# Optimization experiments

Hardware: AMD Instinct MI355X
Metric: run time of the kernel (lower is better)

The kernel has to match this reference:

```python
import jax, jax.numpy as jnp
import numpy as np

B, S, D = 4, 1024, 768
H = 12
DK = D // H            # 64
NUM_EMB = 10
MAX_DIST = 100000.0 * 2 ** 0.5
POS_SCALE = 100000.0   # tile positions live in [0, 100000]


def setup_inputs() -> dict:
    key = jax.random.key(0)
    ks = jax.random.split(key, 12)
    query = jax.random.normal(ks[0], (B, S, D), dtype=jnp.float32)
    key_t = jax.random.normal(ks[1], (B, S, D), dtype=jnp.float32)
    value = jax.random.normal(ks[2], (B, S, D), dtype=jnp.float32)
    tile_positions = jax.random.uniform(ks[3], (B, S, 2), dtype=jnp.float32) * POS_SCALE
    # Linear weights, torch layout [out, in]; xavier_uniform init, zero bias
    lim = float(np.sqrt(6.0 / (D + D)))
    Wq = jax.random.uniform(ks[4], (D, D), minval=-lim, maxval=lim, dtype=jnp.float32)
    Wk = jax.random.uniform(ks[5], (D, D), minval=-lim, maxval=lim, dtype=jnp.float32)
    Wv = jax.random.uniform(ks[6], (D, D), minval=-lim, maxval=lim, dtype=jnp.float32)
    bq = jnp.zeros((D,), jnp.float32)
    bk = jnp.zeros((D,), jnp.float32)
    bv = jnp.zeros((D,), jnp.float32)
    emb_k = jax.random.normal(ks[7], (NUM_EMB, DK), dtype=jnp.float32)  # nn.Embedding default N(0,1)
    return {"query": query, "key": key_t, "value": value,
            "tile_positions": tile_positions,
            "Wq": Wq, "bq": bq, "Wk": Wk, "bk": bk, "Wv": Wv, "bv": bv,
            "emb_k": emb_k}


def reference(query, key, value, tile_positions, Wq, bq, Wk, bk, Wv, bv, emb_k):
    b, s, _ = query.shape
    # projections -> [B, H, S, DK]
    q = (query @ Wq.T + bq).reshape(b, s, H, DK).transpose(0, 2, 1, 3)
    k = (key   @ Wk.T + bk).reshape(b, s, H, DK).transpose(0, 2, 1, 3)
    v = (value @ Wv.T + bv).reshape(b, s, H, DK).transpose(0, 2, 1, 3)
    # pairwise distances, normalized, discretized to embedding indices
    pos = jax.lax.stop_gradient(tile_positions)
    diff = pos[:, :, None, :] - pos[:, None, :, :]          # [B,S,S,2]
    dist = jnp.sqrt(jnp.sum(diff * diff, axis=-1)) / MAX_DIST  # [B,S,S]
    idx = jnp.clip(jnp.round(dist * (NUM_EMB - 1)), 0, NUM_EMB - 1).astype(jnp.int32)
    rk = emb_k[idx]                                          # [B,S,S,DK]
    # logits: QK^T plus distance-aware key bias
    attn_logits = jnp.einsum('bhqd,bhkd->bhqk', q, k)
    attn_logits = attn_logits + jnp.einsum('bhqd,bqkd->bhqk', q, rk)
    attn_logits = attn_logits / (DK ** 0.5)
    attention = jax.nn.softmax(attn_logits, axis=-1)
    out = jnp.einsum('bhqk,bhkd->bhqd', attention, v)       # [B,H,S,DK]
    out = out.transpose(0, 2, 1, 3).reshape(b, s, -1)       # [B,S,D]
    return out
```

## Files before the change

kernel.cpp:

```cpp
#include <hip/hip_runtime.h>
#include <hip/hip_bf16.h>

#define Bsz 4
#define Ssz 1024
#define Dsz 768
#define Hn 12
#define DKsz 64
#define NUMEMB 10

#define IDX_OFF 64
#define K_OFF   4194368
#define V_OFF   10485824
#define WBF_OFF 16777280
#define XBF_OFF 20316224
#define WS_TIER_B 20316224ULL
#define WS_TIER_A 39190592ULL

#define NXz 3145728
#define NWz 589824

#define KVBUF 4096

typedef __attribute__((ext_vector_type(8))) short short8;
typedef __attribute__((ext_vector_type(8))) float float8;
typedef __attribute__((ext_vector_type(4))) float f32x4;
typedef __attribute__((ext_vector_type(4))) unsigned int u32x4;
typedef __attribute__((ext_vector_type(2))) unsigned int u32x2;
typedef __attribute__((ext_vector_type(4))) short s16x4;

__device__ __forceinline__ float bfbits2f(short u) {
    union { unsigned int i; float f; } v;
    v.i = ((unsigned int)(unsigned short)u) << 16;
    return v.f;
}
__device__ __forceinline__ unsigned short f2bf_bits(float f) {
    __hip_bfloat16 h = __float2bfloat16(f);
    return *reinterpret_cast<unsigned short*>(&h);
}

__device__ __forceinline__ int dtvote(const unsigned int* p, int n) {
    int cnt = 0;
    for (int i = (threadIdx.x & 63); i < n; i += 64) {
        const unsigned int ex = (p[i] >> 7) & 0xFF;
        cnt += (ex >= 110 && ex <= 145) ? 1 : 0;
    }
#pragma unroll
    for (int off = 1; off < 64; off <<= 1) cnt += __shfl_xor(cnt, off, 64);
    return (2 * cnt > n) ? 1 : 0;
}

template<bool BF16>
__device__ __forceinline__ float loadf(const void* base, size_t idx) {
    if constexpr (BF16) return __bfloat162float(((const __hip_bfloat16*)base)[idx]);
    else return ((const float*)base)[idx];
}
template<bool BF16>
__device__ __forceinline__ short8 load8bf(const void* base, size_t idx) {
    if constexpr (BF16) {
        return *(const short8*)((const short*)base + idx);
    } else {
        float8 f = *(const float8*)((const float*)base + idx);
        short8 r;
#pragma unroll
        for (int i = 0; i < 8; i++) r[i] = (short)f2bf_bits(f[i]);
        return r;
    }
}
template<bool BF16>
__device__ __forceinline__ float8 load8f(const void* base, size_t idx) {
    if constexpr (BF16) {
        short8 s = *(const short8*)((const short*)base + idx);
        float8 f;
#pragma unroll
        for (int i = 0; i < 8; i++) f[i] = bfbits2f(s[i]);
        return f;
    } else {
        return *(const float8*)((const float*)base + idx);
    }
}

template<bool PB>
__device__ __forceinline__ void idx_body(
    const void* pos, unsigned char* __restrict__ idxb, int kt, int qt, int b)
{
    const int t = threadIdx.x;
    const int r = t >> 2, cc = t & 3;
    const int q = qt * 64 + r;
    const float qx = loadf<PB>(pos, ((size_t)b * Ssz + q) * 2);
    const float qy = loadf<PB>(pos, ((size_t)b * Ssz + q) * 2 + 1);
    const float MAXD = 141421.35623730951f;
    const int k0 = kt * 64 + cc * 16;
    unsigned int w[4];
#pragma unroll
    for (int g = 0; g < 4; g++) {
        unsigned int acc = 0;
#pragma unroll
        for (int u = 0; u < 4; u++) {
            const int k = k0 + g * 4 + u;
            const float kx = loadf<PB>(pos, ((size_t)b * Ssz + k) * 2);
            const float ky = loadf<PB>(pos, ((size_t)b * Ssz + k) * 2 + 1);
            const float dx = __fsub_rn(qx, kx);
            const float dy = __fsub_rn(qy, ky);
            const float ss = __fadd_rn(__fmul_rn(dx, dx), __fmul_rn(dy, dy));
            const float dist = __fdiv_rn(sqrtf(ss), MAXD);
            const float d9 = __fmul_rn(dist, 9.0f);
            int idx = (int)rintf(d9);
            idx = idx < 0 ? 0 : (idx > NUMEMB - 1 ? NUMEMB - 1 : idx);
            acc |= ((unsigned int)idx) << (8 * u);
        }
        w[g] = acc;
    }
    u32x4 v; v[0] = w[0]; v[1] = w[1]; v[2] = w[2]; v[3] = w[3];
    *(u32x4*)(idxb + ((size_t)(b * Ssz + q)) * Ssz + k0) = v;
}

__global__ __launch_bounds__(64) void detect_kernel(
    const unsigned int* __restrict__ q, const unsigned int* __restrict__ p,
    const unsigned int* __restrict__ w, const unsigned int* __restrict__ e,
    int* __restrict__ flags)
{
    const int which = blockIdx.x;
    const unsigned int* ptr = (which == 0) ? q : ((which == 1) ? p : ((which == 2) ? w : e));
    const int n = (which == 3) ? 320 : ((which == 1) ? 4096 : 1024);
    const int f = dtvote(ptr, n);
    if (threadIdx.x == 0) flags[which] = f;
}

__global__ __launch_bounds__(256) void idx_kernel(
    const void* pos, const int* __restrict__ flags, unsigned char* __restrict__ idxb)
{
    if (flags[1] != 0) idx_body<true >(pos, idxb, blockIdx.x, blockIdx.y, blockIdx.z);
    else               idx_body<false>(pos, idxb, blockIdx.x, blockIdx.y, blockIdx.z);
}

__global__ __launch_bounds__(256) void prep_kernel(
    const void* __restrict__ X0, const void* __restrict__ X1, const void* __restrict__ X2,
    const void* __restrict__ W0, const void* __restrict__ W1, const void* __restrict__ W2,
    const void* __restrict__ tpos, const void* __restrict__ emb,
    int* __restrict__ flags, short* __restrict__ Xbf, short* __restrict__ Wbf,
    unsigned char* __restrict__ idxb, int nconv, int doX)
{
    if ((int)blockIdx.x >= nconv) {
        const int i = blockIdx.x - nconv;
        const int kt = i & 15, qt = (i >> 4) & 15, b = i >> 8;
        const int pb = dtvote((const unsigned int*)tpos, 1024);
        if (pb) idx_body<true >(tpos, idxb, kt, qt, b);
        else    idx_body<false>(tpos, idxb, kt, qt, b);
        return;
    }

    if (blockIdx.x == 1) {
        const int f = dtvote((const unsigned int*)tpos, 1024);
        if (threadIdx.x == 0) flags[1] = f;
    } else if (blockIdx.x == 3) {
        const int f = dtvote((const unsigned int*)emb, 320);
        if (threadIdx.x == 0) flags[3] = f;
    }
    const bool xb = dtvote((const unsigned int*)X0, 256) != 0;
    const bool wb = dtvote((const unsigned int*)W0, 256) != 0;
    if (blockIdx.x == 0 && threadIdx.x == 0) { flags[0] = xb ? 1 : 0; flags[2] = wb ? 1 : 0; }

    const long t = (long)blockIdx.x * 256 + threadIdx.x;
    if (doX) {
        const long i8 = t * 8;
        if (i8 < (long)3 * NXz) {
            const int z = (int)(i8 / NXz);
            const long off = i8 - (long)z * NXz;
            const void* X = (z == 0) ? X0 : ((z == 1) ? X1 : X2);
            short8 v = xb ? load8bf<true>(X, off) : load8bf<false>(X, off);
            *(short8*)(Xbf + i8) = v;
        } else {
            const long j = i8 - (long)3 * NXz;
            const int z = (int)(j / NWz);
            const long off = j - (long)z * NWz;
            const void* W = (z == 0) ? W0 : ((z == 1) ? W1 : W2);
            short8 v = wb ? load8bf<true>(W, off) : load8bf<false>(W, off);
            *(short8*)(Wbf + j) = v;
        }
    } else {
        const long j = t * 8;
        const int z = (int)(j / NWz);
        const long off = j - (long)z * NWz;
        const void* W = (z == 0) ? W0 : ((z == 1) ? W1 : W2);
        short8 v = wb ? load8bf<true>(W, off) : load8bf<false>(W, off);
        *(short8*)(Wbf + j) = v;
    }
}

template<bool XB, bool WB>
__device__ __forceinline__ void proj_body(
    const void* X, const void* W, const void* bias, bool biasbf, void* Y, bool ybf,
    int zmode, int bx, int by, short* As, short* Bs)
{
    const int tid  = threadIdx.x;
    const int wave = tid >> 6;
    const int lane = tid & 63;
    const int l15  = lane & 15;
    const int quad = lane >> 4;
    const int wm = wave & 1;
    const int wn = wave >> 1;
    const int m0 = bx * 64;
    const int n0 = by * 128;

    f32x4 acc[2][4];
#pragma unroll
    for (int i = 0; i < 2; i++)
#pragma unroll
        for (int j = 0; j < 4; j++) acc[i][j] = (f32x4)0.0f;

    const int r0 = tid >> 3;
    const int cc = tid & 7;

    short8 pa0 = load8bf<XB>(X, (size_t)(m0 + r0)      * Dsz + cc * 8);
    short8 pa1 = load8bf<XB>(X, (size_t)(m0 + 32 + r0) * Dsz + cc * 8);
    short8 pb0 = load8bf<WB>(W, (size_t)(n0 + r0)      * Dsz + cc * 8);
    short8 pb1 = load8bf<WB>(W, (size_t)(n0 + 32 + r0) * Dsz + cc * 8);
    short8 pb2 = load8bf<WB>(W, (size_t)(n0 + 64 + r0) * Dsz + cc * 8);
    short8 pb3 = load8bf<WB>(W, (size_t)(n0 + 96 + r0) * Dsz + cc * 8);

    for (int kk = 0; kk < Dsz; kk += 64) {
        __syncthreads();
        *(short8*)&As[(r0)      * 72 + cc * 8] = pa0;
        *(short8*)&As[(32 + r0) * 72 + cc * 8] = pa1;
        *(short8*)&Bs[(r0)      * 72 + cc * 8] = pb0;
        *(short8*)&Bs[(32 + r0) * 72 + cc * 8] = pb1;
        *(short8*)&Bs[(64 + r0) * 72 + cc * 8] = pb2;
        *(short8*)&Bs[(96 + r0) * 72 + cc * 8] = pb3;
        __syncthreads();

        if (kk + 64 < Dsz) {
            const int k2 = kk + 64 + cc * 8;
            pa0 = load8bf<XB>(X, (size_t)(m0 + r0)      * Dsz + k2);
            pa1 = load8bf<XB>(X, (size_t)(m0 + 32 + r0) * Dsz + k2);
            pb0 = load8bf<WB>(W, (size_t)(n0 + r0)      * Dsz + k2);
            pb1 = load8bf<WB>(W, (size_t)(n0 + 32 + r0) * Dsz + k2);
            pb2 = load8bf<WB>(W, (size_t)(n0 + 64 + r0) * Dsz + k2);
            pb3 = load8bf<WB>(W, (size_t)(n0 + 96 + r0) * Dsz + k2);
        }

#pragma unroll
        for (int st = 0; st < 2; st++) {
            short8 af[2], bf[4];
#pragma unroll
            for (int i = 0; i < 2; i++)
                af[i] = *(const short8*)&As[(wm * 32 + i * 16 + l15) * 72 + st * 32 + quad * 8];
#pragma unroll
            for (int j = 0; j < 4; j++)
                bf[j] = *(const short8*)&Bs[(wn * 64 + j * 16 + l15) * 72 + st * 32 + quad * 8];
#pragma unroll
            for (int i = 0; i < 2; i++)
#pragma unroll
                for (int j = 0; j < 4; j++)
                    acc[i][j] = __builtin_amdgcn_mfma_f32_16x16x32_bf16(af[i], bf[j], acc[i][j], 0, 0, 0);
        }
    }

#pragma unroll
    for (int j = 0; j < 4; j++) {
        const int n = n0 + wn * 64 + j * 16 + l15;
        const float bv_ = biasbf ? loadf<true>(bias, n) : loadf<false>(bias, n);
        const int hh = n >> 6, dk = n & 63;
#pragma unroll
        for (int i = 0; i < 2; i++) {
            const int ms = m0 + wm * 32 + i * 16 + quad * 4;
            const int bb = ms >> 10;
            const int s0 = ms & 1023;
            if (zmode == 2) {
                s16x4 pkv;
#pragma unroll
                for (int r = 0; r < 4; r++) pkv[r] = (short)f2bf_bits(acc[i][j][r] + bv_);
                *(s16x4*)((short*)Y + (((size_t)bb * Hn + hh) * DKsz + dk) * Ssz + s0) = pkv;
            } else if (zmode == 1) {
#pragma unroll
                for (int r = 0; r < 4; r++)
                    ((__hip_bfloat16*)Y)[(((size_t)bb * Hn + hh) * Ssz + (s0 + r)) * DKsz + dk] =
                        __float2bfloat16(acc[i][j][r] + bv_);
            } else {
#pragma unroll
                for (int r = 0; r < 4; r++) {
                    const float val = acc[i][j][r] + bv_;
                    const size_t oi = (size_t)(ms + r) * Dsz + n;
                    if (ybf) ((__hip_bfloat16*)Y)[oi] = __float2bfloat16(val);
                    else     ((float*)Y)[oi] = val;
                }
            }
        }
    }
}

__global__ __launch_bounds__(256) void proj_kernel(
    const void* X0, const void* X1, const void* X2,
    const void* Wq, const void* bq, const void* Wk, const void* bk,
    const void* Wv, const void* bv,
    void* Qw, void* Kw, void* Vw, const int* __restrict__ flags,
    int fx, int fw)
{
    __shared__ __align__(16) short As[64 * 72];
    __shared__ __align__(16) short Bs[128 * 72];
    const int z = blockIdx.z;
    const void* X = (z == 0) ? X0 : ((z == 1) ? X1 : X2);
    const void* W = (z == 0) ? Wq : ((z == 1) ? Wk : Wv);
    const void* B = (z == 0) ? bq : ((z == 1) ? bk : bv);
    void* Y = (z == 0) ? Qw : ((z == 1) ? Kw : Vw);
    const bool xb = fx || flags[0] != 0;
    const bool wb = fw || flags[2] != 0;
    const bool biasbf = flags[2] != 0;
    const bool ybf = (flags[0] != 0) || (z != 0);
    if (xb) { if (wb) proj_body<true , true >(X, W, B, biasbf, Y, ybf, z, blockIdx.x, blockIdx.y, As, Bs);
              else    proj_body<true , false>(X, W, B, biasbf, Y, ybf, z, blockIdx.x, blockIdx.y, As, Bs); }
    else    { if (wb) proj_body<false, true >(X, W, B, biasbf, Y, ybf, z, blockIdx.x, blockIdx.y, As, Bs);
              else    proj_body<false, false>(X, W, B, biasbf, Y, ybf, z, blockIdx.x, blockIdx.y, As, Bs); }
}

template<bool QB, bool EB>
__device__ __forceinline__ void attn_body(
    const void* Qw, const short* __restrict__ Ks, const short* __restrict__ Vs,
    const unsigned char* __restrict__ idxb, const void* __restrict__ emb, void* out,
    unsigned short* Klds, unsigned short* Vtlds, float* qe)
{
    const int qt = blockIdx.x, h = blockIdx.y, b = blockIdx.z;
    const int tid  = threadIdx.x;
    const int wave = tid >> 6;
    const int lane = tid & 63;
    const int l15  = lane & 15;
    const int quad = lane >> 4;

    const float CSC = 0.18033688011112042f;

    for (int p = tid; p < 64 * NUMEMB; p += 256) {
        const int row = p / NUMEMB, e = p - row * NUMEMB;
        const size_t qoff = ((size_t)b * Ssz + qt * 64 + row) * Dsz + h * DKsz;
        float s = 0.f;
#pragma unroll
        for (int c = 0; c < 8; c++) {
            short8 qv = load8bf<QB>(Qw, qoff + c * 8);
            float8 ef = load8f<EB>(emb, (size_t)e * DKsz + c * 8);
#pragma unroll
            for (int i = 0; i < 8; i++) s += bfbits2f(qv[i]) * ef[i];
        }
        qe[p] = s * CSC;
    }

    short8 qfrag[2];
    {
        const size_t qbase = ((size_t)b * Ssz + qt * 64 + wave * 16 + l15) * Dsz + h * DKsz;
        qfrag[0] = load8bf<QB>(Qw, qbase + quad * 8);
        qfrag[1] = load8bf<QB>(Qw, qbase + 32 + quad * 8);
    }

    float m_run = -1e30f, l_run = 0.f;
    f32x4 oacc[4];
#pragma unroll
    for (int j = 0; j < 4; j++) oacc[j] = (f32x4)0.0f;

    const int r0 = tid >> 3, cc = tid & 7;
    const int swr   = (r0 & 3) | (((r0 >> 3) & 1) << 2);
    const int wroff = r0 * 64 + (cc ^ swr) * 8;

    const int swk = (l15 & 3) | (((l15 >> 2) & 1) << 2);
    const int vsw = (l15 & 3) | (((l15 >> 3) & 1) << 2);
    int koff[4][2];
#pragma unroll
    for (int jb = 0; jb < 4; jb++) {
        const int krow = (jb & 2) * 16 + (l15 >> 2) * 8 + (jb & 1) * 4 + (l15 & 3);
#pragma unroll
        for (int st = 0; st < 2; st++)
            koff[jb][st] = krow * 64 + ((st * 4 + quad) ^ swk) * 8;
    }
    int voff[2];
#pragma unroll
    for (int st = 0; st < 2; st++) voff[st] = ((st * 4 + quad) ^ vsw) * 8;

    const short* kp = Ks + ((size_t)(b * Hn + h) * Ssz) * DKsz + tid * 8;
    const short* vp = Vs + ((size_t)(b * Hn + h) * DKsz + r0) * Ssz + cc * 8;
    const unsigned char* ip = idxb + ((size_t)b * Ssz + qt * 64 + wave * 16 + l15) * Ssz + quad * 8;
    const int qrow10 = (wave * 16 + l15) * NUMEMB;

    short8 pk0 = *(const short8*)(kp);
    short8 pk1 = *(const short8*)(kp + 2048);
    short8 pv0 = *(const short8*)(vp);
    short8 pv1 = *(const short8*)(vp + 32 * Ssz);
    u32x2 idA = *(const u32x2*)(ip);
    u32x2 idB = *(const u32x2*)(ip + 32);

    *(short8*)&Klds[wroff]            = pk0;
    *(short8*)&Klds[32 * 64 + wroff]  = pk1;
    *(short8*)&Vtlds[wroff]           = pv0;
    *(short8*)&Vtlds[32 * 64 + wroff] = pv1;
    __syncthreads();

    for (int it = 0; it < 16; ++it) {
        const int cur = (it & 1) * KVBUF;
        const int nxt = cur ^ KVBUF;
        const unsigned int jd[4] = { idA[0], idA[1], idB[0], idB[1] };

        if (it + 1 < 16) {
            kp += 4096;
            vp += 64;
            ip += 64;
            pk0 = *(const short8*)(kp);
            pk1 = *(const short8*)(kp + 2048);
            pv0 = *(const short8*)(vp);
            pv1 = *(const short8*)(vp + 32 * Ssz);
            idA = *(const u32x2*)(ip);
            idB = *(const u32x2*)(ip + 32);
        }

        f32x4 sf[4];
#pragma unroll
        for (int jb = 0; jb < 4; jb++) sf[jb] = (f32x4)0.0f;
        __builtin_amdgcn_s_setprio(1);
#pragma unroll
        for (int st = 0; st < 2; st++) {
#pragma unroll
            for (int jb = 0; jb < 4; jb++) {
                short8 kf = *(const short8*)&Klds[cur + koff[jb][st]];
                sf[jb] = __builtin_amdgcn_mfma_f32_16x16x32_bf16(kf, qfrag[st], sf[jb], 0, 0, 0);
            }
        }
        __builtin_amdgcn_s_setprio(0);

        float sv[4][4];
#pragma unroll
        for (int jb = 0; jb < 4; jb++) {
            const unsigned int iw = jd[jb];
#pragma unroll
            for (int r = 0; r < 4; r++)
                sv[jb][r] = fmaf(sf[jb][r], CSC, qe[qrow10 + ((iw >> (8 * r)) & 0xFF)]);
        }

        float t0 = fmaxf(fmaxf(sv[0][0], sv[0][1]), fmaxf(sv[0][2], sv[0][3]));
        float t1 = fmaxf(fmaxf(sv[1][0], sv[1][1]), fmaxf(sv[1][2], sv[1][3]));
        float t2 = fmaxf(fmaxf(sv[2][0], sv[2][1]), fmaxf(sv[2][2], sv[2][3]));
        float t3 = fmaxf(fmaxf(sv[3][0], sv[3][1]), fmaxf(sv[3][2], sv[3][3]));
        float vmax = fmaxf(fmaxf(t0, t1), fmaxf(t2, t3));
        vmax = fmaxf(vmax, __shfl_xor(vmax, 16, 64));
        vmax = fmaxf(vmax, __shfl_xor(vmax, 32, 64));

        if (!__all(vmax - m_run <= 8.0f)) {
            const float mnew = fmaxf(m_run, vmax);
            const float alpha = exp2f(m_run - mnew);
            m_run = mnew;
            l_run *= alpha;
            float aO[4];
#pragma unroll
            for (int r = 0; r < 4; r++)
                aO[r] = __shfl(alpha, (lane & 48) | (quad * 4 + r), 64);
#pragma unroll
            for (int j = 0; j < 4; j++) {
                f32x4 o = oacc[j];
#pragma unroll
                for (int r = 0; r < 4; r++) o[r] *= aO[r];
                oacc[j] = o;
            }
        }

#pragma unroll
        for (int jb = 0; jb < 4; jb++)
#pragma unroll
            for (int r = 0; r < 4; r++)
                sv[jb][r] = exp2f(sv[jb][r] - m_run);

        float s0 = (sv[0][0] + sv[0][1]) + (sv[0][2] + sv[0][3]);
        float s1 = (sv[1][0] + sv[1][1]) + (sv[1][2] + sv[1][3]);
        float s2 = (sv[2][0] + sv[2][1]) + (sv[2][2] + sv[2][3]);
        float s3 = (sv[3][0] + sv[3][1]) + (sv[3][2] + sv[3][3]);
        float psum = (s0 + s1) + (s2 + s3);
        psum += __shfl_xor(psum, 16, 64);
        psum += __shfl_xor(psum, 32, 64);
        l_run += psum;

        short8 pa[2];
#pragma unroll
        for (int st = 0; st < 2; st++)
#pragma unroll
            for (int j = 0; j < 8; j++)
                pa[st][j] = (short)f2bf_bits(sv[2 * st + (j >> 2)][j & 3]);

        __builtin_amdgcn_s_setprio(1);
#pragma unroll
        for (int st = 0; st < 2; st++) {
#pragma unroll
            for (int j = 0; j < 4; j++) {
                short8 vb = *(const short8*)&Vtlds[cur + (j * 16 + l15) * 64 + voff[st]];
                oacc[j] = __builtin_amdgcn_mfma_f32_16x16x32_bf16(pa[st], vb, oacc[j], 0, 0, 0);
            }
        }
        __builtin_amdgcn_s_setprio(0);

        if (it + 1 < 16) {
            *(short8*)&Klds[nxt + wroff]            = pk0;
            *(short8*)&Klds[nxt + 32 * 64 + wroff]  = pk1;
            *(short8*)&Vtlds[nxt + wroff]           = pv0;
            *(short8*)&Vtlds[nxt + 32 * 64 + wroff] = pv1;
        }
        __syncthreads();
    }

    const float inv = 1.0f / l_run;
    float invO[4];
#pragma unroll
    for (int r = 0; r < 4; r++)
        invO[r] = __shfl(inv, (lane & 48) | (quad * 4 + r), 64);

#pragma unroll
    for (int r = 0; r < 4; r++) {
        const int m = qt * 64 + wave * 16 + quad * 4 + r;
#pragma unroll
        for (int j = 0; j < 4; j++) {
            const int n = h * DKsz + j * 16 + l15;
            const float val = oacc[j][r] * invO[r];
            const size_t oidx = ((size_t)b * Ssz + m) * Dsz + n;
            if constexpr (QB) ((__hip_bfloat16*)out)[oidx] = __float2bfloat16(val);
            else              ((float*)out)[oidx] = val;
        }
    }
}

__global__ __launch_bounds__(256) void attn_kernel(
    const void* Qw, const short* __restrict__ Ks, const short* __restrict__ Vs,
    const unsigned char* __restrict__ idxb, const void* __restrict__ emb, void* out,
    const int* __restrict__ flags)
{
    __shared__ __align__(16) unsigned short Klds[2 * KVBUF];
    __shared__ __align__(16) unsigned short Vtlds[2 * KVBUF];
    __shared__ __align__(16) float qe[64 * NUMEMB];

    const bool qb = flags[0] != 0, eb = flags[3] != 0;
    if (qb) { if (eb) attn_body<true , true >(Qw, Ks, Vs, idxb, emb, out, Klds, Vtlds, qe);
              else    attn_body<true , false>(Qw, Ks, Vs, idxb, emb, out, Klds, Vtlds, qe); }
    else    { if (eb) attn_body<false, true >(Qw, Ks, Vs, idxb, emb, out, Klds, Vtlds, qe);
              else    attn_body<false, false>(Qw, Ks, Vs, idxb, emb, out, Klds, Vtlds, qe); }
}

extern "C" void kernel_launch(void* const* d_in, const int* in_sizes, int n_in,
                              void* d_out, int out_size, void* d_ws, size_t ws_size,
                              hipStream_t stream) {
    const void* query = d_in[0];
    const void* key   = d_in[1];
    const void* value = d_in[2];
    const void* tpos  = d_in[3];
    const void* Wq    = d_in[4];
    const void* bq    = d_in[5];
    const void* Wk    = d_in[6];
    const void* bk    = d_in[7];
    const void* Wv    = d_in[8];
    const void* bv    = d_in[9];
    const void* emb   = d_in[10];

    int*           flags = (int*)d_ws;
    unsigned char* idxb  = (unsigned char*)d_ws + IDX_OFF;
    void*          Kw    = (char*)d_ws + K_OFF;
    void*          Vw    = (char*)d_ws + V_OFF;
    short*         Wbf   = (short*)((char*)d_ws + WBF_OFF);
    short*         Xbf   = (short*)((char*)d_ws + XBF_OFF);
    void*          Qw    = d_out;

    const bool tierA = ws_size >= WS_TIER_A;
    const bool tierB = !tierA && ws_size >= WS_TIER_B;

    if (tierA) {
        prep_kernel<<<5472 + 1024, 256, 0, stream>>>(
            query, key, value, Wq, Wk, Wv, tpos, emb,
            flags, Xbf, Wbf, idxb, 5472, 1);
        proj_kernel<<<dim3(64, 6, 3), 256, 0, stream>>>(
            Xbf, Xbf + NXz, Xbf + 2 * NXz,
            Wbf, bq, Wbf + NWz, bk, Wbf + 2 * NWz, bv,
            Qw, Kw, Vw, flags, 1, 1);
    } else if (tierB) {
        prep_kernel<<<864 + 1024, 256, 0, stream>>>(
            query, key, value, Wq, Wk, Wv, tpos, emb,
            flags, Xbf, Wbf, idxb, 864, 0);
        proj_kernel<<<dim3(64, 6, 3), 256, 0, stream>>>(
            query, key, value,
            Wbf, bq, Wbf + NWz, bk, Wbf + 2 * NWz, bv,
            Qw, Kw, Vw, flags, 0, 1);
    } else {
        detect_kernel<<<4, 64, 0, stream>>>(
            (const unsigned int*)query, (const unsigned int*)tpos,
            (const unsigned int*)Wq, (const unsigned int*)emb, flags);
        idx_kernel<<<dim3(16, 16, Bsz), 256, 0, stream>>>(tpos, flags, idxb);
        proj_kernel<<<dim3(64, 6, 3), 256, 0, stream>>>(
            query, key, value, Wq, bq, Wk, bk, Wv, bv,
            Qw, Kw, Vw, flags, 0, 0);
    }

    attn_kernel<<<dim3(16, Hn, Bsz), 256, 0, stream>>>(
        Qw, (const short*)Kw, (const short*)Vw, idxb, emb, d_out, flags);
}
```

Measured before the change: 201.4 us.

## Enlarge attention query tile to 128 rows with 512-thread blocks

Each attention block now covers 128 query rows using 8 waves and 512 threads, which halves the grid. Every K/V tile staged in shared memory is therefore reused by twice as many query rows, and each thread issues one K and one V load per iteration instead of two. The cost is fewer blocks for the GPU, less parallelism, and heavier register pressure under the 512-thread launch bound. The code still uses `tid>>3` row mapping with 512 threads, so r0 now spans 0..63, and the K/V tile layout must remain consistent with that mapping.

```diff
diff --git a/kernel.cpp b/kernel.cpp
--- a/kernel.cpp
+++ b/kernel.cpp
@@ -20,6 +20,7 @@
 #define NWz 589824
 
 #define KVBUF 4096
+#define QBLK 128
 
 typedef __attribute__((ext_vector_type(8))) short short8;
 typedef __attribute__((ext_vector_type(8))) float float8;
@@ -327,9 +328,9 @@
 
     const float CSC = 0.18033688011112042f;
 
-    for (int p = tid; p < 64 * NUMEMB; p += 256) {
+    for (int p = tid; p < QBLK * NUMEMB; p += 512) {
         const int row = p / NUMEMB, e = p - row * NUMEMB;
-        const size_t qoff = ((size_t)b * Ssz + qt * 64 + row) * Dsz + h * DKsz;
+        const size_t qoff = ((size_t)b * Ssz + qt * QBLK + row) * Dsz + h * DKsz;
         float s = 0.f;
 #pragma unroll
         for (int c = 0; c < 8; c++) {
@@ -343,7 +344,7 @@
 
     short8 qfrag[2];
     {
-        const size_t qbase = ((size_t)b * Ssz + qt * 64 + wave * 16 + l15) * Dsz + h * DKsz;
+        const size_t qbase = ((size_t)b * Ssz + qt * QBLK + wave * 16 + l15) * Dsz + h * DKsz;
         qfrag[0] = load8bf<QB>(Qw, qbase + quad * 8);
         qfrag[1] = load8bf<QB>(Qw, qbase + 32 + quad * 8);
     }
@@ -373,20 +374,16 @@
 
     const short* kp = Ks + ((size_t)(b * Hn + h) * Ssz) * DKsz + tid * 8;
     const short* vp = Vs + ((size_t)(b * Hn + h) * DKsz + r0) * Ssz + cc * 8;
-    const unsigned char* ip = idxb + ((size_t)b * Ssz + qt * 64 + wave * 16 + l15) * Ssz + quad * 8;
+    const unsigned char* ip = idxb + ((size_t)b * Ssz + qt * QBLK + wave * 16 + l15) * Ssz + quad * 8;
     const int qrow10 = (wave * 16 + l15) * NUMEMB;
 
-    short8 pk0 = *(const short8*)(kp);
-    short8 pk1 = *(const short8*)(kp + 2048);
-    short8 pv0 = *(const short8*)(vp);
-    short8 pv1 = *(const short8*)(vp + 32 * Ssz);
+    short8 pk = *(const short8*)(kp);
+    short8 pv = *(const short8*)(vp);
     u32x2 idA = *(const u32x2*)(ip);
     u32x2 idB = *(const u32x2*)(ip + 32);
 
-    *(short8*)&Klds[wroff]            = pk0;
-    *(short8*)&Klds[32 * 64 + wroff]  = pk1;
-    *(short8*)&Vtlds[wroff]           = pv0;
-    *(short8*)&Vtlds[32 * 64 + wroff] = pv1;
+    *(short8*)&Klds[wroff]  = pk;
+    *(short8*)&Vtlds[wroff] = pv;
     __syncthreads();
 
     for (int it = 0; it < 16; ++it) {
@@ -398,10 +395,8 @@
             kp += 4096;
             vp += 64;
             ip += 64;
-            pk0 = *(const short8*)(kp);
-            pk1 = *(const short8*)(kp + 2048);
-            pv0 = *(const short8*)(vp);
-            pv1 = *(const short8*)(vp + 32 * Ssz);
+            pk = *(const short8*)(kp);
+            pv = *(const short8*)(vp);
             idA = *(const u32x2*)(ip);
             idB = *(const u32x2*)(ip + 32);
         }
@@ -489,10 +484,8 @@
         __builtin_amdgcn_s_setprio(0);
 
         if (it + 1 < 16) {
-            *(short8*)&Klds[nxt + wroff]            = pk0;
-            *(short8*)&Klds[nxt + 32 * 64 + wroff]  = pk1;
-            *(short8*)&Vtlds[nxt + wroff]           = pv0;
-            *(short8*)&Vtlds[nxt + 32 * 64 + wroff] = pv1;
+            *(short8*)&Klds[nxt + wroff]  = pk;
+            *(short8*)&Vtlds[nxt + wroff] = pv;
         }
         __syncthreads();
     }
@@ -505,7 +498,7 @@
 
 #pragma unroll
     for (int r = 0; r < 4; r++) {
-        const int m = qt * 64 + wave * 16 + quad * 4 + r;
+        const int m = qt * QBLK + wave * 16 + quad * 4 + r;
 #pragma unroll
         for (int j = 0; j < 4; j++) {
             const int n = h * DKsz + j * 16 + l15;
@@ -517,14 +510,14 @@
     }
 }
 
-__global__ __launch_bounds__(256) void attn_kernel(
+__global__ __launch_bounds__(512) void attn_kernel(
     const void* Qw, const short* __restrict__ Ks, const short* __restrict__ Vs,
     const unsigned char* __restrict__ idxb, const void* __restrict__ emb, void* out,
     const int* __restrict__ flags)
 {
     __shared__ __align__(16) unsigned short Klds[2 * KVBUF];
     __shared__ __align__(16) unsigned short Vtlds[2 * KVBUF];
-    __shared__ __align__(16) float qe[64 * NUMEMB];
+    __shared__ __align__(16) float qe[QBLK * NUMEMB];
 
     const bool qb = flags[0] != 0, eb = flags[3] != 0;
     if (qb) { if (eb) attn_body<true , true >(Qw, Ks, Vs, idxb, emb, out, Klds, Vtlds, qe);
@@ -585,6 +578,6 @@
             Qw, Kw, Vw, flags, 0, 0);
     }
 
-    attn_kernel<<<dim3(16, Hn, Bsz), 256, 0, stream>>>(
+    attn_kernel<<<dim3(Ssz / QBLK, Hn, Bsz), 512, 0, stream>>>(
         Qw, (const short*)Kw, (const short*)Vw, idxb, emb, d_out, flags);
 }
```

Result: slower. 207.6 us (+3.1%).
